# Kernel optimization log

Hardware: AMD Instinct MI355X
Metric: run time of the kernel (lower is better)

The kernel has to match this reference:

```python
import jax, jax.numpy as jnp
import numpy as np

# init_kwargs: zs (sorted list of supported atomic numbers)
ZS = jnp.array([0, 1, 6, 7, 8, 11, 13, 14, 16, 17, 26, 29, 47, 78, 79, 83], dtype=jnp.float32)

N_ATOMS = 8_000_000


def setup_inputs() -> dict:
    key = jax.random.key(0)
    # integer-valued atomic numbers in [0, 83); float dtype so gradients exist
    z = jax.random.randint(key, (N_ATOMS,), 0, 83).astype(jnp.float32)
    return {"atomic_numbers": z}


def reference(atomic_numbers):
    K = ZS.shape[0]
    # first index j with ZS[j] >= z (vectorized replacement of the python loop)
    j = jnp.clip(jnp.searchsorted(ZS, atomic_numbers, side="left"), 0, K - 1)
    z_hi = ZS[j]
    exact = z_hi == atomic_numbers           # one-hot branch: z in zs
    j_lo = jnp.clip(j - 1, 0, K - 1)
    z_lo = ZS[j_lo]
    denom = jnp.where(exact, 1.0, z_hi - z_lo)   # safe divide when j_lo == j
    w_hi = jnp.where(exact, 1.0, (atomic_numbers - z_lo) / denom)
    w_lo = jnp.where(exact, 0.0, (z_hi - atomic_numbers) / denom)
    # fused one-hot/interpolation write: [N, K]
    encoded = (w_hi[:, None] * jax.nn.one_hot(j, K, dtype=jnp.float32)
               + w_lo[:, None] * jax.nn.one_hot(j_lo, K, dtype=jnp.float32))
    return encoded
```

## Files before the change

### kernel.cpp

```cpp
#include <hip/hip_runtime.h>


#define K_TAB 16
#define N_Z   83
#define WSZ   64
#define CA    256
#define INNER (CA / 16)

typedef float v4f __attribute__((ext_vector_type(4)));

__global__ __launch_bounds__(WSZ) void node_encode_kernel(
    const float* __restrict__ z_in,
    float* __restrict__ out,
    int n_atoms, int n_chunks)
{
    __shared__ float lut[N_Z][K_TAB];
    __shared__ float zl[2][CA];

    const int lane = threadIdx.x;

    constexpr float tab[K_TAB] = {0.f, 1.f, 6.f, 7.f, 8.f, 11.f, 13.f, 14.f,
                                  16.f, 17.f, 26.f, 29.f, 47.f, 78.f, 79.f, 83.f};
    for (int row = lane; row < N_Z; row += WSZ) {
        const float zf = (float)row;
        int j = 0;
        float zlo = tab[0];
        float zhi = tab[K_TAB - 1];
#pragma unroll
        for (int k = 0; k < K_TAB; ++k) {
            const bool lt = (tab[k] < zf);
            j += lt ? 1 : 0;
            zlo = lt ? tab[k] : zlo;
        }
#pragma unroll
        for (int k = K_TAB - 2; k >= 0; --k) {
            zhi = (tab[k] >= zf) ? tab[k] : zhi;
        }
        const bool exact = (zhi == zf);
        const float denom = exact ? 1.f : (zhi - zlo);
        const float inv   = 1.f / denom;
        const float whi   = exact ? 1.f : (zf - zlo) * inv;
        const float wlo   = exact ? 0.f : (zhi - zf) * inv;
        int jl = j - (exact ? 0 : 1);
        if (jl < 0) jl = 0;
#pragma unroll
        for (int c = 0; c < K_TAB; ++c) {
            lut[row][c] = (c == j ? whi : 0.f) + (c == jl ? wlo : 0.f);
        }
    }

    v4f* __restrict__ out4 = reinterpret_cast<v4f*>(out);
    const int nwaves = gridDim.x;
    const int gwave  = blockIdx.x;

    int c = gwave;
    v4f zreg = {0.f, 0.f, 0.f, 0.f};
    if (c < n_chunks) {
        const int a0 = c * CA + lane * 4;
        if (a0 + 3 < n_atoms) {
            zreg = *reinterpret_cast<const v4f*>(&z_in[a0]);
        } else {
#pragma unroll
            for (int e = 0; e < 4; ++e)
                if (a0 + e < n_atoms) zreg[e] = z_in[a0 + e];
        }
    }

    int p = 0;
    for (; c < n_chunks; c += nwaves, ++p) {
        *reinterpret_cast<v4f*>(&zl[p & 1][lane * 4]) = zreg;

        const int cn = c + nwaves;
        if (cn < n_chunks) {
            const int a0 = cn * CA + lane * 4;
            if (a0 + 3 < n_atoms) {
                zreg = *reinterpret_cast<const v4f*>(&z_in[a0]);
            } else {
                v4f zt = {0.f, 0.f, 0.f, 0.f};
#pragma unroll
                for (int e = 0; e < 4; ++e)
                    if (a0 + e < n_atoms) zt[e] = z_in[a0 + e];
                zreg = zt;
            }
        }

        const float* __restrict__ zb = zl[p & 1];
        const long base4 = (long)c * (CA * 4);
        if ((c + 1) * CA <= n_atoms) {
#pragma unroll
            for (int k = 0; k < INNER; ++k) {
                const int u  = k * WSZ + lane;
                const int zi = (int)zb[u >> 2];
                const v4f v  = *reinterpret_cast<const v4f*>(&lut[zi][(u & 3) << 2]);
                out4[base4 + u] = v;
            }
        } else {
            const long total4 = (long)n_atoms * 4;
            for (int k = 0; k < INNER; ++k) {
                const int u = k * WSZ + lane;
                const long g = base4 + u;
                if (g < total4) {
                    const int zi = (int)zb[u >> 2];
                    out4[g] = *reinterpret_cast<const v4f*>(&lut[zi][(u & 3) << 2]);
                }
            }
        }
    }
}

extern "C" void kernel_launch(void* const* d_in, const int* in_sizes, int n_in,
                              void* d_out, int out_size, void* d_ws, size_t ws_size,
                              hipStream_t stream) {
    const float* z = (const float*)d_in[0];
    float* out = (float*)d_out;
    const int n_atoms = in_sizes[0];

    const int n_chunks = (n_atoms + CA - 1) / CA;
    const int grid = 1024;

    node_encode_kernel<<<grid, WSZ, 0, stream>>>(z, out, n_atoms, n_chunks);
}
```

Baseline: 105.0 us.

## Replace shared LUT with per-atom computed interpolation params in shared memory

Drops the per-block 83x16 lookup table, which had to be built at kernel start. Each lane now computes the interpolation weight and the two packed indices for its four atoms and stores them in a double-buffered shared array. Output vectors are then synthesized with compares and selects. This removes the table setup and the dependent LDS gather, at the cost of more ALU work per atom. The kernel is store-bandwidth bound writing 512 MB, so any gain is likely small. Computing wlo as 1-whi may differ in the last bits from the reference.

```diff
diff --git a/kernel.cpp b/kernel.cpp
--- a/kernel.cpp
+++ b/kernel.cpp
@@ -2,108 +2,140 @@
 
 
 #define K_TAB 16
-#define N_Z   83
 #define WSZ   64
 #define CA    256
 #define INNER (CA / 16)
 
 typedef float v4f __attribute__((ext_vector_type(4)));
 
+__device__ __forceinline__ float2 atom_params(float z) {
+    constexpr float tab[K_TAB] = {0.f, 1.f, 6.f, 7.f, 8.f, 11.f, 13.f, 14.f,
+                                  16.f, 17.f, 26.f, 29.f, 47.f, 78.f, 79.f, 83.f};
+    int j = 0;
+    float zlo = tab[0];
+    float zhi = tab[K_TAB - 1];
+#pragma unroll
+    for (int k = 0; k < K_TAB; ++k) {
+        const bool lt = (tab[k] < z);
+        j += lt ? 1 : 0;
+        zlo = lt ? tab[k] : zlo;
+    }
+#pragma unroll
+    for (int k = K_TAB - 2; k >= 0; --k) {
+        zhi = (tab[k] >= z) ? tab[k] : zhi;
+    }
+    if (j > K_TAB - 1) j = K_TAB - 1;
+    const bool exact = (zhi == z);
+    const float denom = exact ? 1.f : (zhi - zlo);
+    const float whi   = exact ? 1.f : (z - zlo) / denom;
+    int jl = j - (exact ? 0 : 1);
+    if (jl < 0) jl = 0;
+    float2 r;
+    r.x = whi;
+    r.y = __uint_as_float((unsigned)j | ((unsigned)jl << 8));
+    return r;
+}
+
+__device__ __forceinline__ v4f load_z4(const float* __restrict__ z_in,
+                                       int c, int lane, int n_atoms) {
+    const int a0 = c * CA + lane * 4;
+    v4f r = {0.f, 0.f, 0.f, 0.f};
+    if (a0 + 3 < n_atoms) {
+        r = *reinterpret_cast<const v4f*>(&z_in[a0]);
+    } else {
+#pragma unroll
+        for (int e = 0; e < 4; ++e)
+            if (a0 + e < n_atoms) r[e] = z_in[a0 + e];
+    }
+    return r;
+}
+
+__device__ __forceinline__ void publish_params(float2* __restrict__ pmbuf,
+                                               int lane, v4f zv) {
+    const float2 q0 = atom_params(zv[0]);
+    const float2 q1 = atom_params(zv[1]);
+    const float2 q2 = atom_params(zv[2]);
+    const float2 q3 = atom_params(zv[3]);
+    v4f w0, w1;
+    w0.x = q0.x; w0.y = q0.y; w0.z = q1.x; w0.w = q1.y;
+    w1.x = q2.x; w1.y = q2.y; w1.z = q3.x; w1.w = q3.y;
+    v4f* dst = reinterpret_cast<v4f*>(&pmbuf[lane * 4]);
+    dst[0] = w0;
+    dst[1] = w1;
+}
+
 __global__ __launch_bounds__(WSZ) void node_encode_kernel(
     const float* __restrict__ z_in,
     float* __restrict__ out,
     int n_atoms, int n_chunks)
 {
-    __shared__ float lut[N_Z][K_TAB];
-    __shared__ float zl[2][CA];
+    __shared__ float2 pm[2][CA];
 
-    const int lane = threadIdx.x;
-
-    constexpr float tab[K_TAB] = {0.f, 1.f, 6.f, 7.f, 8.f, 11.f, 13.f, 14.f,
-                                  16.f, 17.f, 26.f, 29.f, 47.f, 78.f, 79.f, 83.f};
-    for (int row = lane; row < N_Z; row += WSZ) {
-        const float zf = (float)row;
-        int j = 0;
-        float zlo = tab[0];
-        float zhi = tab[K_TAB - 1];
-#pragma unroll
-        for (int k = 0; k < K_TAB; ++k) {
-            const bool lt = (tab[k] < zf);
-            j += lt ? 1 : 0;
-            zlo = lt ? tab[k] : zlo;
-        }
-#pragma unroll
-        for (int k = K_TAB - 2; k >= 0; --k) {
-            zhi = (tab[k] >= zf) ? tab[k] : zhi;
-        }
-        const bool exact = (zhi == zf);
-        const float denom = exact ? 1.f : (zhi - zlo);
-        const float inv   = 1.f / denom;
-        const float whi   = exact ? 1.f : (zf - zlo) * inv;
-        const float wlo   = exact ? 0.f : (zhi - zf) * inv;
-        int jl = j - (exact ? 0 : 1);
-        if (jl < 0) jl = 0;
-#pragma unroll
-        for (int c = 0; c < K_TAB; ++c) {
-            lut[row][c] = (c == j ? whi : 0.f) + (c == jl ? wlo : 0.f);
-        }
-    }
-
-    v4f* __restrict__ out4 = reinterpret_cast<v4f*>(out);
+    const int lane   = threadIdx.x;
     const int nwaves = gridDim.x;
     const int gwave  = blockIdx.x;
 
+    v4f* __restrict__ out4 = reinterpret_cast<v4f*>(out);
+
     int c = gwave;
-    v4f zreg = {0.f, 0.f, 0.f, 0.f};
     if (c < n_chunks) {
-        const int a0 = c * CA + lane * 4;
-        if (a0 + 3 < n_atoms) {
-            zreg = *reinterpret_cast<const v4f*>(&z_in[a0]);
-        } else {
-#pragma unroll
-            for (int e = 0; e < 4; ++e)
-                if (a0 + e < n_atoms) zreg[e] = z_in[a0 + e];
-        }
+        const v4f z0 = load_z4(z_in, c, lane, n_atoms);
+        publish_params(pm[0], lane, z0);
     }
 
     int p = 0;
     for (; c < n_chunks; c += nwaves, ++p) {
-        *reinterpret_cast<v4f*>(&zl[p & 1][lane * 4]) = zreg;
+        const int cn = c + nwaves;
+        const bool haveN = (cn < n_chunks);
+        v4f zregN = {0.f, 0.f, 0.f, 0.f};
+        if (haveN) zregN = load_z4(z_in, cn, lane, n_atoms);
 
-        const int cn = c + nwaves;
-        if (cn < n_chunks) {
-            const int a0 = cn * CA + lane * 4;
-            if (a0 + 3 < n_atoms) {
-                zreg = *reinterpret_cast<const v4f*>(&z_in[a0]);
-            } else {
-                v4f zt = {0.f, 0.f, 0.f, 0.f};
-#pragma unroll
-                for (int e = 0; e < 4; ++e)
-                    if (a0 + e < n_atoms) zt[e] = z_in[a0 + e];
-                zreg = zt;
-            }
-        }
-
-        const float* __restrict__ zb = zl[p & 1];
+        const float2* __restrict__ pmb = pm[p & 1];
         const long base4 = (long)c * (CA * 4);
+        const int  c0    = (lane & 3) << 2;
         if ((c + 1) * CA <= n_atoms) {
 #pragma unroll
             for (int k = 0; k < INNER; ++k) {
-                const int u  = k * WSZ + lane;
-                const int zi = (int)zb[u >> 2];
-                const v4f v  = *reinterpret_cast<const v4f*>(&lut[zi][(u & 3) << 2]);
-                out4[base4 + u] = v;
+                const float2 pp = pmb[k * 16 + (lane >> 2)];
+                const float whi = pp.x;
+                const unsigned d = __float_as_uint(pp.y);
+                const int j  = d & 0xFF;
+                const int jl = (d >> 8) & 0xFF;
+                const float wlo = 1.f - whi;
+                const int rj = j - c0;
+                const int rl = jl - c0;
+                v4f v;
+                v.x = (rj == 0 ? whi : 0.f) + (rl == 0 ? wlo : 0.f);
+                v.y = (rj == 1 ? whi : 0.f) + (rl == 1 ? wlo : 0.f);
+                v.z = (rj == 2 ? whi : 0.f) + (rl == 2 ? wlo : 0.f);
+                v.w = (rj == 3 ? whi : 0.f) + (rl == 3 ? wlo : 0.f);
+                out4[base4 + k * WSZ + lane] = v;
             }
         } else {
             const long total4 = (long)n_atoms * 4;
             for (int k = 0; k < INNER; ++k) {
-                const int u = k * WSZ + lane;
-                const long g = base4 + u;
+                const long g = base4 + k * WSZ + lane;
                 if (g < total4) {
-                    const int zi = (int)zb[u >> 2];
-                    out4[g] = *reinterpret_cast<const v4f*>(&lut[zi][(u & 3) << 2]);
+                    const float2 pp = pmb[k * 16 + (lane >> 2)];
+                    const float whi = pp.x;
+                    const unsigned d = __float_as_uint(pp.y);
+                    const int j  = d & 0xFF;
+                    const int jl = (d >> 8) & 0xFF;
+                    const float wlo = 1.f - whi;
+                    const int rj = j - c0;
+                    const int rl = jl - c0;
+                    v4f v;
+                    v.x = (rj == 0 ? whi : 0.f) + (rl == 0 ? wlo : 0.f);
+                    v.y = (rj == 1 ? whi : 0.f) + (rl == 1 ? wlo : 0.f);
+                    v.z = (rj == 2 ? whi : 0.f) + (rl == 2 ? wlo : 0.f);
+                    v.w = (rj == 3 ? whi : 0.f) + (rl == 3 ? wlo : 0.f);
+                    out4[g] = v;
                 }
             }
+        }
+
+        if (haveN) {
+            publish_params(pm[(p + 1) & 1], lane, zregN);
         }
     }
 }
```

Result: slower. 132.7 us (+26.4%).
